# Performance work log

Measured on AMD Instinct MI355X. Metric: run time of the kernel, lower is better.

## Reference

```python
import jax, jax.numpy as jnp
import numpy as np

D_IN = 1024
D_OUT = 1024

def setup_inputs() -> dict:
    key = jax.random.key(0)
    kx, kq, kk, kv = jax.random.split(key, 4)
    x = jax.random.normal(kx, (4, 4096, D_IN), dtype=jnp.float32)
    s = 1.0 / np.sqrt(D_IN)
    Wq = jax.random.uniform(kq, (D_IN, D_OUT), dtype=jnp.float32, minval=-s, maxval=s)
    Wk = jax.random.uniform(kk, (D_IN, D_OUT), dtype=jnp.float32, minval=-s, maxval=s)
    Wv = jax.random.uniform(kv, (D_IN, D_OUT), dtype=jnp.float32, minval=-s, maxval=s)
    return {"x": x, "Wq": Wq, "Wk": Wk, "Wv": Wv}

def reference(x, Wq, Wk, Wv):
    # x: [B, S, d_in]; single-head causal attention (dropout p=0 => identity)
    B, S, _ = x.shape
    Q = jnp.einsum('bsd,de->bse', x, Wq)
    K = jnp.einsum('bsd,de->bse', x, Wk)
    V = jnp.einsum('bsd,de->bse', x, Wv)
    scale = 1.0 / jnp.sqrt(jnp.asarray(K.shape[-1], dtype=Q.dtype))
    scores = jnp.einsum('bqe,bke->bqk', Q, K) * scale  # [B, S, S]
    causal = jnp.tril(jnp.ones((S, S), dtype=bool))     # mask upper triangle (diag=1)
    scores = jnp.where(causal, scores, -jnp.inf)
    weights = jax.nn.softmax(scores, axis=-1)
    return jnp.einsum('bqk,bke->bqe', weights, V)
```

## Files before the change

### kernel.cpp

```cpp
#include <hip/hip_runtime.h>
#include <hip/hip_bf16.h>
#include <stdint.h>

typedef short short8 __attribute__((ext_vector_type(8)));
typedef short short4v __attribute__((ext_vector_type(4)));
typedef float f32x4 __attribute__((ext_vector_type(4)));

static __device__ __forceinline__ short f2bf(float f) {
  union { float f; uint32_t u; } v; v.f = f;
  uint32_t r = (v.u + 0x7fffu + ((v.u >> 16) & 1u)) >> 16;
  return (short)(uint16_t)r;
}
static __device__ __forceinline__ float bf2f(short h) {
  union { uint32_t u; float f; } v; v.u = ((uint32_t)(uint16_t)h) << 16;
  return v.f;
}

#define MFMA(a, b, c) __builtin_amdgcn_mfma_f32_16x16x32_bf16((a), (b), (c), 0, 0, 0)

static __device__ __forceinline__ void gload16(const short* g, short* l) {
  __builtin_amdgcn_global_load_lds(
      (const __attribute__((address_space(1))) void*)g,
      (__attribute__((address_space(3))) void*)l, 16, 0, 0);
}

static __device__ __forceinline__ void gemm256_pipe(
    const short* __restrict__ Ag, int lda,
    const short* __restrict__ Bg, int ldb, int kext,
    short* lds, int t, f32x4 (&acc)[8][4])
{
  const int w = t >> 6, lane = t & 63;
  const int lr = lane & 15, lk = lane >> 4;
  const int wm = w >> 2, wn = w & 3;
  const int nk = kext >> 6;

  const int sr0 = t >> 3;          const int sc0 = (t & 7) ^ (sr0 & 7);
  const int sr1 = (512 + t) >> 3;  const int sc1 = (t & 7) ^ (sr1 & 7);
  const int ch0 = (lk ^ (lr & 7)) * 8;
  const int ch1 = ((4 + lk) ^ (lr & 7)) * 8;

#pragma unroll
  for (int h = 0; h < 2; ++h) {
    gload16(Ag + (size_t)(h * 128 + sr0) * lda + sc0 * 8, lds + h * 8192 + w * 512);
    gload16(Ag + (size_t)(h * 128 + sr1) * lda + sc1 * 8, lds + h * 8192 + 4096 + w * 512);
    gload16(Bg + (size_t)(h * 128 + sr0) * ldb + sc0 * 8, lds + 32768 + h * 8192 + w * 512);
    gload16(Bg + (size_t)(h * 128 + sr1) * ldb + sc1 * 8, lds + 32768 + h * 8192 + 4096 + w * 512);
  }
  asm volatile("s_waitcnt vmcnt(0)" ::: "memory");
  __builtin_amdgcn_s_barrier();

  for (int g = 0; g < nk; ++g) {
    short* Ac = lds + ((g & 1) << 14);
    short* Bc = lds + 32768 + ((g & 1) << 14);
    short* An = lds + (((g + 1) & 1) << 14);
    short* Bn = lds + 32768 + (((g + 1) & 1) << 14);
    const int kk = (g + 1) << 6;
    const bool st = (g + 1 < nk);

    short8 bfr[4][2];
#pragma unroll
    for (int q = 0; q < 4; ++q) {
      short8 af[2][2];
#pragma unroll
      for (int mtl = 0; mtl < 2; ++mtl) {
        const int rbase = (wm * 128 + (2 * q + mtl) * 16 + lr) * 64;
        af[mtl][0] = *(const short8*)&Ac[rbase + ch0];
        af[mtl][1] = *(const short8*)&Ac[rbase + ch1];
      }
      if (q == 0) {
#pragma unroll
        for (int nt = 0; nt < 4; ++nt) {
          const int rbase = (wn * 64 + nt * 16 + lr) * 64;
          bfr[nt][0] = *(const short8*)&Bc[rbase + ch0];
          bfr[nt][1] = *(const short8*)&Bc[rbase + ch1];
        }
      }
      if (st && q == 0) {
#pragma unroll
        for (int h = 0; h < 2; ++h) {
          gload16(Ag + (size_t)(h * 128 + sr0) * lda + kk + sc0 * 8, An + h * 8192 + w * 512);
          gload16(Ag + (size_t)(h * 128 + sr1) * lda + kk + sc1 * 8, An + h * 8192 + 4096 + w * 512);
        }
      }
      if (st && q == 1) {
#pragma unroll
        for (int h = 0; h < 2; ++h) {
          gload16(Bg + (size_t)(h * 128 + sr0) * ldb + kk + sc0 * 8, Bn + h * 8192 + w * 512);
          gload16(Bg + (size_t)(h * 128 + sr1) * ldb + kk + sc1 * 8, Bn + h * 8192 + 4096 + w * 512);
        }
      }
      __builtin_amdgcn_s_barrier();
      asm volatile("s_waitcnt lgkmcnt(0)" ::: "memory");
      __builtin_amdgcn_sched_barrier(0);
      __builtin_amdgcn_s_setprio(1);
#pragma unroll
      for (int kh = 0; kh < 2; ++kh)
#pragma unroll
        for (int mtl = 0; mtl < 2; ++mtl)
#pragma unroll
          for (int nt = 0; nt < 4; ++nt)
            acc[2 * q + mtl][nt] = MFMA(af[mtl][kh], bfr[nt][kh], acc[2 * q + mtl][nt]);
      __builtin_amdgcn_s_setprio(0);
      if (q == 3) asm volatile("s_waitcnt vmcnt(0)" ::: "memory");
      __builtin_amdgcn_s_barrier();
    }
  }
}

static __device__ __forceinline__ void gemm_tile128(
    const short* __restrict__ Ag, int lda,
    const short* __restrict__ Bg, int ldb, int kext,
    short* Alds, short* Blds, int w, int lane, f32x4 (&acc)[4][4])
{
  const int wr = (w >> 1) * 64, wc = (w & 1) * 64;
  const int lr = lane & 15, lk = lane >> 4;

  const int c0 = w * 128 + lane;
  const int c1 = c0 + 64;
  const int r0 = c0 >> 2, cg0 = (c0 & 3) ^ ((r0 >> 1) & 3);
  const int r1 = c1 >> 2, cg1 = (c1 & 3) ^ ((r1 >> 1) & 3);
  const short* a0 = Ag + (size_t)r0 * lda + cg0 * 8;
  const short* a1 = Ag + (size_t)r1 * lda + cg1 * 8;
  const short* b0 = Bg + (size_t)r0 * ldb + cg0 * 8;
  const short* b1 = Bg + (size_t)r1 * ldb + cg1 * 8;
  short* la0 = Alds + w * 1024;
  short* la1 = la0 + 512;
  short* lb0 = Blds + w * 1024;
  short* lb1 = lb0 + 512;

  int ra[4], rb[4];
#pragma unroll
  for (int mt = 0; mt < 4; ++mt) {
    int rl = wr + mt * 16 + lr;
    ra[mt] = rl * 32 + (lk ^ ((rl >> 1) & 3)) * 8;
  }
#pragma unroll
  for (int nt = 0; nt < 4; ++nt) {
    int rl = wc + nt * 16 + lr;
    rb[nt] = rl * 32 + (lk ^ ((rl >> 1) & 3)) * 8;
  }

  for (int kk = 0; kk < kext; kk += 32) {
    if (kk) __syncthreads();
    gload16(a0 + kk, la0);
    gload16(a1 + kk, la1);
    gload16(b0 + kk, lb0);
    gload16(b1 + kk, lb1);
    __syncthreads();
    short8 af[4], bfr[4];
#pragma unroll
    for (int mt = 0; mt < 4; ++mt) af[mt] = *(const short8*)&Alds[ra[mt]];
#pragma unroll
    for (int nt = 0; nt < 4; ++nt) bfr[nt] = *(const short8*)&Blds[rb[nt]];
#pragma unroll
    for (int mt = 0; mt < 4; ++mt)
#pragma unroll
      for (int nt = 0; nt < 4; ++nt)
        acc[mt][nt] = MFMA(af[mt], bfr[nt], acc[mt][nt]);
  }
}

__global__ __launch_bounds__(256)
void cvt_x(const float* __restrict__ x, short* __restrict__ xb) {
  size_t i = (size_t)blockIdx.x * 256 + threadIdx.x;
  f32x4 a = *(const f32x4*)(x + i * 8);
  f32x4 b = *(const f32x4*)(x + i * 8 + 4);
  short8 h = { f2bf(a.x), f2bf(a.y), f2bf(a.z), f2bf(a.w),
               f2bf(b.x), f2bf(b.y), f2bf(b.z), f2bf(b.w) };
  *(short8*)(xb + i * 8) = h;
}

__global__ __launch_bounds__(256)
void cvt_w(const float* __restrict__ Wq, const float* __restrict__ Wk,
           const float* __restrict__ Wv, short* __restrict__ wt) {
  __shared__ short Tl[128][136];
  const int z = blockIdx.z;
  const float* W = (z == 0) ? Wq : (z == 1) ? Wk : Wv;
  const float scale = (z == 0) ? 0.03125f : 1.0f;
  const int c0 = blockIdx.x * 128, r0 = blockIdx.y * 128;
  const int t = threadIdx.x;
#pragma unroll
  for (int j = 0; j < 16; ++j) {
    int id = j * 256 + t;
    int row = id >> 5, c4 = id & 31;
    f32x4 v = *(const f32x4*)(W + (size_t)(r0 + row) * 1024 + c0 + c4 * 4);
#pragma unroll
    for (int cc = 0; cc < 4; ++cc) Tl[c4 * 4 + cc][row] = f2bf(v[cc] * scale);
  }
  __syncthreads();
  short* dst = wt + (size_t)z * 1048576;
#pragma unroll
  for (int j = 0; j < 8; ++j) {
    int id = j * 256 + t;
    int col = id >> 4, r8 = id & 15;
    *(short8*)(dst + (size_t)(c0 + col) * 1024 + r0 + r8 * 8) =
        *(const short8*)&Tl[col][r8 * 8];
  }
}

__global__ __launch_bounds__(512, 2)
void qkv_gemm(const short* __restrict__ xb, const short* __restrict__ wt,
              short* __restrict__ q, short* __restrict__ k,
              short* __restrict__ vt) {
  extern __shared__ short lds[];
  const int z = blockIdx.z;
  const int n0 = blockIdx.x * 256, m0 = blockIdx.y * 256;
  const int t = threadIdx.x;
  f32x4 acc[8][4] = {};
  gemm256_pipe(xb + (size_t)m0 * 1024, 1024,
               wt + (size_t)z * 1048576 + (size_t)n0 * 1024, 1024, 1024,
               lds, t, acc);
  const int w = t >> 6, lane = t & 63;
  const int lr = lane & 15, lk = lane >> 4;
  const int wm = w >> 2, wn = w & 3;
#pragma unroll
  for (int mt = 0; mt < 8; ++mt) {
#pragma unroll
    for (int nt = 0; nt < 4; ++nt) {
      int col = n0 + wn * 64 + nt * 16 + lr;
      int rbase = m0 + wm * 128 + mt * 16 + lk * 4;
      if (z == 2) {
        int bb = rbase >> 12, s = rbase & 4095;
        short4v h = { f2bf(acc[mt][nt][0]), f2bf(acc[mt][nt][1]),
                      f2bf(acc[mt][nt][2]), f2bf(acc[mt][nt][3]) };
        *(short4v*)(vt + ((size_t)bb * 1024 + col) * 4096 + s) = h;
      } else {
        short* dst = (z == 0) ? q : k;
#pragma unroll
        for (int i = 0; i < 4; ++i)
          dst[(size_t)(rbase + i) * 1024 + col] = f2bf(acc[mt][nt][i]);
      }
    }
  }
}

__global__ __launch_bounds__(512, 2)
void s_gemm(const short* __restrict__ q, const short* __restrict__ k,
            short* __restrict__ P, float* __restrict__ lpart) {
  extern __shared__ short lds[];
  const int bid = blockIdx.x;
  const int b = bid & 3, tt = bid >> 2;
  int ti = (int)((sqrtf(8.f * tt + 1.f) - 1.f) * 0.5f);
  while ((ti + 1) * (ti + 2) / 2 <= tt) ++ti;
  while (ti * (ti + 1) / 2 > tt) --ti;
  const int tj = tt - ti * (ti + 1) / 2;
  const int t = threadIdx.x;
  f32x4 acc[8][4] = {};
  gemm256_pipe(q + ((size_t)(b * 4096 + ti * 256)) * 1024, 1024,
               k + ((size_t)(b * 4096 + tj * 256)) * 1024, 1024, 1024,
               lds, t, acc);
  const int w = t >> 6, lane = t & 63;
  const int lr = lane & 15, lk = lane >> 4;
  const int wm = w >> 2, wn = w & 3;
  const bool diag = (ti == tj);
#pragma unroll
  for (int mt = 0; mt < 8; ++mt) {
#pragma unroll
    for (int i = 0; i < 4; ++i) {
      const int rl = wm * 128 + mt * 16 + lk * 4 + i;
      size_t prow = ((size_t)(b * 4096 + ti * 256 + rl)) * 4096 + tj * 256;
      float rs = 0.f;
#pragma unroll
      for (int nt = 0; nt < 4; ++nt) {
        const int cl = wn * 64 + nt * 16 + lr;
        float e = (!diag || cl <= rl) ? __expf(acc[mt][nt][i]) : 0.f;
        short pb = f2bf(e);
        P[prow + cl] = pb;
        rs += bf2f(pb);
      }
      rs += __shfl_xor(rs, 1);
      rs += __shfl_xor(rs, 2);
      rs += __shfl_xor(rs, 4);
      rs += __shfl_xor(rs, 8);
      if (lr == 0)
        lpart[((size_t)(tj * 4 + wn)) * 16384 + b * 4096 + ti * 256 + rl] = rs;
    }
  }
}

__global__ __launch_bounds__(256)
void l_reduce(const float* __restrict__ lpart, float* __restrict__ lsum) {
  int idx = blockIdx.x * 256 + threadIdx.x;
  int qq = idx & 4095;
  int ti = qq >> 8;
  float s = 0.f;
  for (int tj = 0; tj <= ti; ++tj) {
#pragma unroll
    for (int e = 0; e < 4; ++e)
      s += lpart[(size_t)(tj * 4 + e) * 16384 + idx];
  }
  lsum[idx] = s;
}

__global__ __launch_bounds__(256)
void pv_gemm(const short* __restrict__ P, const short* __restrict__ vt,
             const float* __restrict__ lsum, float* __restrict__ out) {
  __shared__ short Alds[128 * 32], Blds[128 * 32];
  const int bid = blockIdx.x;
  const int b = bid & 3;
  const int r = bid >> 2;
  const int dt = r & 7;
  const int qt = 31 - (r >> 3);
  const int t = threadIdx.x, w = t >> 6, lane = t & 63;
  f32x4 acc[4][4] = {};
  gemm_tile128(P + ((size_t)(b * 4096 + qt * 128)) * 4096, 4096,
               vt + ((size_t)(b * 1024 + dt * 128)) * 4096, 4096,
               (qt + 1) * 128, Alds, Blds, w, lane, acc);
  const int lr = lane & 15, lk = lane >> 4;
  const int wr = (w >> 1) * 64, wc = (w & 1) * 64;
#pragma unroll
  for (int mt = 0; mt < 4; ++mt) {
#pragma unroll
    for (int i = 0; i < 4; ++i) {
      int rl = wr + mt * 16 + lk * 4 + i;
      int grow = b * 4096 + qt * 128 + rl;
      float inv = 1.0f / lsum[grow];
#pragma unroll
      for (int nt = 0; nt < 4; ++nt) {
        int cl = wc + nt * 16 + lr;
        out[(size_t)grow * 1024 + dt * 128 + cl] = acc[mt][nt][i] * inv;
      }
    }
  }
}

extern "C" void kernel_launch(void* const* d_in, const int* in_sizes, int n_in,
                              void* d_out, int out_size, void* d_ws, size_t ws_size,
                              hipStream_t stream) {
  (void)in_sizes; (void)n_in; (void)out_size; (void)ws_size;
  const float* x  = (const float*)d_in[0];
  const float* Wq = (const float*)d_in[1];
  const float* Wk = (const float*)d_in[2];
  const float* Wv = (const float*)d_in[3];
  float* out = (float*)d_out;

  short* q_ws  = (short*)d_ws;
  short* k_ws  = q_ws + (size_t)16777216;
  short* vt_ws = k_ws + (size_t)16777216;
  short* P     = vt_ws + (size_t)16777216;
  short* xb    = P;
  float* lpart = (float*)(P + (size_t)67108864);
  float* lsum  = lpart + (size_t)64 * 16384;
  short* wt    = (short*)(lsum + 16384);

  const int gemm_lds = 131072;
  hipFuncSetAttribute((const void*)qkv_gemm,
                      hipFuncAttributeMaxDynamicSharedMemorySize, gemm_lds);
  hipFuncSetAttribute((const void*)s_gemm,
                      hipFuncAttributeMaxDynamicSharedMemorySize, gemm_lds);

  cvt_x<<<dim3(8192), 256, 0, stream>>>(x, xb);
  cvt_w<<<dim3(8, 8, 3), 256, 0, stream>>>(Wq, Wk, Wv, wt);
  qkv_gemm<<<dim3(4, 64, 3), 512, gemm_lds, stream>>>(xb, wt, q_ws, k_ws, vt_ws);
  s_gemm<<<dim3(544), 512, gemm_lds, stream>>>(q_ws, k_ws, P, lpart);
  l_reduce<<<dim3(64), 256, 0, stream>>>(lpart, lsum);
  pv_gemm<<<dim3(1024), 256, 0, stream>>>(P, vt_ws, lsum, out);
}
```

Measured before the change: 340.2 us.

## Replace double-buffered K=64 GEMM pipeline with 4-slot K=32 ring buffer

The 256x256 GEMM mainloop now steps K in chunks of 32 and keeps a 4-slot LDS ring with loads issued three stages ahead, instead of double-buffering 64-wide K chunks. It uses a different XOR swizzle for the 32-wide rows and fine-grained vmcnt waits, so global loads stay in flight longer and barrier stalls on memory latency should drop. The cost is more barriers per unit of K (two phases per 32-K step) and less MFMA work between synchronisations.

```diff
diff --git a/kernel.cpp b/kernel.cpp
--- a/kernel.cpp
+++ b/kernel.cpp
@@ -24,7 +24,7 @@
       (__attribute__((address_space(3))) void*)l, 16, 0, 0);
 }
 
-static __device__ __forceinline__ void gemm256_pipe(
+static __device__ __forceinline__ void gemm256_ring(
     const short* __restrict__ Ag, int lda,
     const short* __restrict__ Bg, int ldb, int kext,
     short* lds, int t, f32x4 (&acc)[8][4])
@@ -32,78 +32,86 @@
   const int w = t >> 6, lane = t & 63;
   const int lr = lane & 15, lk = lane >> 4;
   const int wm = w >> 2, wn = w & 3;
-  const int nk = kext >> 6;
-
-  const int sr0 = t >> 3;          const int sc0 = (t & 7) ^ (sr0 & 7);
-  const int sr1 = (512 + t) >> 3;  const int sc1 = (t & 7) ^ (sr1 & 7);
-  const int ch0 = (lk ^ (lr & 7)) * 8;
-  const int ch1 = ((4 + lk) ^ (lr & 7)) * 8;
-
-#pragma unroll
-  for (int h = 0; h < 2; ++h) {
-    gload16(Ag + (size_t)(h * 128 + sr0) * lda + sc0 * 8, lds + h * 8192 + w * 512);
-    gload16(Ag + (size_t)(h * 128 + sr1) * lda + sc1 * 8, lds + h * 8192 + 4096 + w * 512);
-    gload16(Bg + (size_t)(h * 128 + sr0) * ldb + sc0 * 8, lds + 32768 + h * 8192 + w * 512);
-    gload16(Bg + (size_t)(h * 128 + sr1) * ldb + sc1 * 8, lds + 32768 + h * 8192 + 4096 + w * 512);
-  }
-  asm volatile("s_waitcnt vmcnt(0)" ::: "memory");
+  const int nk = kext >> 5;
+
+  const int i0 = t, i1 = 512 + t;
+  const int r0 = i0 >> 2, c0 = (i0 & 3) ^ ((r0 >> 1) & 3);
+  const int r1 = i1 >> 2, c1 = (i1 & 3) ^ ((r1 >> 1) & 3);
+  const short* a0 = Ag + (size_t)r0 * lda + c0 * 8;
+  const short* a1 = Ag + (size_t)r1 * lda + c1 * 8;
+  const short* b0 = Bg + (size_t)r0 * ldb + c0 * 8;
+  const short* b1 = Bg + (size_t)r1 * ldb + c1 * 8;
+  const int chq = (lk ^ ((lr >> 1) & 3)) * 8;
+
+#pragma unroll
+  for (int p = 0; p < 3; ++p) {
+    short* slot = lds + p * 16384;
+    gload16(a0 + p * 32, slot + w * 512);
+    gload16(a1 + p * 32, slot + 4096 + w * 512);
+    gload16(b0 + p * 32, slot + 8192 + w * 512);
+    gload16(b1 + p * 32, slot + 12288 + w * 512);
+  }
+  asm volatile("s_waitcnt vmcnt(8)" ::: "memory");
   __builtin_amdgcn_s_barrier();
 
-  for (int g = 0; g < nk; ++g) {
-    short* Ac = lds + ((g & 1) << 14);
-    short* Bc = lds + 32768 + ((g & 1) << 14);
-    short* An = lds + (((g + 1) & 1) << 14);
-    short* Bn = lds + 32768 + (((g + 1) & 1) << 14);
-    const int kk = (g + 1) << 6;
-    const bool st = (g + 1 < nk);
-
-    short8 bfr[4][2];
-#pragma unroll
-    for (int q = 0; q < 4; ++q) {
-      short8 af[2][2];
-#pragma unroll
-      for (int mtl = 0; mtl < 2; ++mtl) {
-        const int rbase = (wm * 128 + (2 * q + mtl) * 16 + lr) * 64;
-        af[mtl][0] = *(const short8*)&Ac[rbase + ch0];
-        af[mtl][1] = *(const short8*)&Ac[rbase + ch1];
-      }
-      if (q == 0) {
-#pragma unroll
-        for (int nt = 0; nt < 4; ++nt) {
-          const int rbase = (wn * 64 + nt * 16 + lr) * 64;
-          bfr[nt][0] = *(const short8*)&Bc[rbase + ch0];
-          bfr[nt][1] = *(const short8*)&Bc[rbase + ch1];
-        }
-      }
-      if (st && q == 0) {
-#pragma unroll
-        for (int h = 0; h < 2; ++h) {
-          gload16(Ag + (size_t)(h * 128 + sr0) * lda + kk + sc0 * 8, An + h * 8192 + w * 512);
-          gload16(Ag + (size_t)(h * 128 + sr1) * lda + kk + sc1 * 8, An + h * 8192 + 4096 + w * 512);
-        }
-      }
-      if (st && q == 1) {
-#pragma unroll
-        for (int h = 0; h < 2; ++h) {
-          gload16(Bg + (size_t)(h * 128 + sr0) * ldb + kk + sc0 * 8, Bn + h * 8192 + w * 512);
-          gload16(Bg + (size_t)(h * 128 + sr1) * ldb + kk + sc1 * 8, Bn + h * 8192 + 4096 + w * 512);
-        }
-      }
-      __builtin_amdgcn_s_barrier();
-      asm volatile("s_waitcnt lgkmcnt(0)" ::: "memory");
-      __builtin_amdgcn_sched_barrier(0);
-      __builtin_amdgcn_s_setprio(1);
-#pragma unroll
-      for (int kh = 0; kh < 2; ++kh)
-#pragma unroll
-        for (int mtl = 0; mtl < 2; ++mtl)
-#pragma unroll
-          for (int nt = 0; nt < 4; ++nt)
-            acc[2 * q + mtl][nt] = MFMA(af[mtl][kh], bfr[nt][kh], acc[2 * q + mtl][nt]);
-      __builtin_amdgcn_s_setprio(0);
-      if (q == 3) asm volatile("s_waitcnt vmcnt(0)" ::: "memory");
-      __builtin_amdgcn_s_barrier();
-    }
+  for (int tt = 0; tt < nk; ++tt) {
+    short* slot  = lds + (tt & 3) * 16384;
+    short* nslot = lds + ((tt + 3) & 3) * 16384;
+    const int kk = (tt + 3) << 5;
+    const bool st = (tt + 3) < nk;
+    short8 bfr[4];
+
+    short8 af[4];
+#pragma unroll
+    for (int mt = 0; mt < 4; ++mt) {
+      int rl = wm * 128 + mt * 16 + lr;
+      af[mt] = *(const short8*)&slot[rl * 32 + chq];
+    }
+#pragma unroll
+    for (int nt = 0; nt < 4; ++nt) {
+      int rl = wn * 64 + nt * 16 + lr;
+      bfr[nt] = *(const short8*)&slot[8192 + rl * 32 + chq];
+    }
+    if (st) {
+      gload16(a0 + kk, nslot + w * 512);
+      gload16(a1 + kk, nslot + 4096 + w * 512);
+    }
+    __builtin_amdgcn_s_barrier();
+    asm volatile("s_waitcnt lgkmcnt(0)" ::: "memory");
+    __builtin_amdgcn_sched_barrier(0);
+    __builtin_amdgcn_s_setprio(1);
+#pragma unroll
+    for (int mt = 0; mt < 4; ++mt)
+#pragma unroll
+      for (int nt = 0; nt < 4; ++nt)
+        acc[mt][nt] = MFMA(af[mt], bfr[nt], acc[mt][nt]);
+    __builtin_amdgcn_s_setprio(0);
+    __builtin_amdgcn_s_barrier();
+
+#pragma unroll
+    for (int mt = 0; mt < 4; ++mt) {
+      int rl = wm * 128 + (4 + mt) * 16 + lr;
+      af[mt] = *(const short8*)&slot[rl * 32 + chq];
+    }
+    if (st) {
+      gload16(b0 + kk, nslot + 8192 + w * 512);
+      gload16(b1 + kk, nslot + 12288 + w * 512);
+    }
+    __builtin_amdgcn_s_barrier();
+    asm volatile("s_waitcnt lgkmcnt(0)" ::: "memory");
+    __builtin_amdgcn_sched_barrier(0);
+    __builtin_amdgcn_s_setprio(1);
+#pragma unroll
+    for (int mt = 0; mt < 4; ++mt)
+#pragma unroll
+      for (int nt = 0; nt < 4; ++nt)
+        acc[4 + mt][nt] = MFMA(af[mt], bfr[nt], acc[4 + mt][nt]);
+    __builtin_amdgcn_s_setprio(0);
+    const int rem = nk - 1 - tt;
+    if (rem >= 3)      { asm volatile("s_waitcnt vmcnt(8)" ::: "memory"); }
+    else if (rem == 2) { asm volatile("s_waitcnt vmcnt(4)" ::: "memory"); }
+    else if (rem == 1) { asm volatile("s_waitcnt vmcnt(0)" ::: "memory"); }
+    __builtin_amdgcn_s_barrier();
   }
 }
 
@@ -207,7 +215,7 @@
   const int n0 = blockIdx.x * 256, m0 = blockIdx.y * 256;
   const int t = threadIdx.x;
   f32x4 acc[8][4] = {};
-  gemm256_pipe(xb + (size_t)m0 * 1024, 1024,
+  gemm256_ring(xb + (size_t)m0 * 1024, 1024,
                wt + (size_t)z * 1048576 + (size_t)n0 * 1024, 1024, 1024,
                lds, t, acc);
   const int w = t >> 6, lane = t & 63;
@@ -246,7 +254,7 @@
   const int tj = tt - ti * (ti + 1) / 2;
   const int t = threadIdx.x;
   f32x4 acc[8][4] = {};
-  gemm256_pipe(q + ((size_t)(b * 4096 + ti * 256)) * 1024, 1024,
+  gemm256_ring(q + ((size_t)(b * 4096 + ti * 256)) * 1024, 1024,
                k + ((size_t)(b * 4096 + tj * 256)) * 1024, 1024, 1024,
                lds, t, acc);
   const int w = t >> 6, lane = t & 63;
```

Result: slower. 353.4 us (+3.9%).
